# Kernel optimization log

Measured on AMD Instinct MI355X. Metric: run time of the kernel, lower is better.

Reference implementation:

```python
import jax, jax.numpy as jnp
import numpy as np

D_MODEL = 1024
NUM_HEADS = 16
SEQ_LEN = 4096
DEPTH = D_MODEL // NUM_HEADS


def setup_inputs() -> dict:
    key = jax.random.key(0)
    ks = jax.random.split(key, 11)
    sp = 1.0 / np.sqrt(D_MODEL)
    return {
        "q": jax.random.normal(ks[0], (SEQ_LEN, D_MODEL), jnp.float32),
        "k": jax.random.normal(ks[1], (SEQ_LEN, D_MODEL), jnp.float32),
        "v": jax.random.normal(ks[2], (SEQ_LEN, D_MODEL), jnp.float32),
        "Wq": jax.random.normal(ks[3], (D_MODEL, D_MODEL), jnp.float32) * sp,
        "bq": jax.random.normal(ks[4], (D_MODEL,), jnp.float32) * 0.02,
        "Wk": jax.random.normal(ks[5], (D_MODEL, D_MODEL), jnp.float32) * sp,
        "bk": jax.random.normal(ks[6], (D_MODEL,), jnp.float32) * 0.02,
        "Wv": jax.random.normal(ks[7], (D_MODEL, D_MODEL), jnp.float32) * sp,
        "bv": jax.random.normal(ks[8], (D_MODEL,), jnp.float32) * 0.02,
        "Wo": jax.random.normal(ks[9], (D_MODEL, D_MODEL), jnp.float32) * sp,
        "bo": jax.random.normal(ks[10], (D_MODEL,), jnp.float32) * 0.02,
    }


def _split_heads(x):
    # [S, D] -> [H, S, depth], matching torch reshape + permute(1,0,2)
    s = x.shape[0]
    return jnp.transpose(x.reshape(s, NUM_HEADS, DEPTH), (1, 0, 2))


def reference(q, k, v, Wq, bq, Wk, bk, Wv, bv, Wo, bo):
    # Linear projections (weights stored so that y = x @ W + b)
    qh = _split_heads(q @ Wq + bq)  # [H, S, d]
    kh = _split_heads(k @ Wk + bk)
    vh = _split_heads(v @ Wv + bv)
    scale = 1.0 / jnp.sqrt(jnp.asarray(DEPTH, qh.dtype))
    scores = jnp.einsum("hqd,hkd->hqk", qh, kh) * scale  # [H, S, S]
    attn = jax.nn.softmax(scores, axis=-1)
    vals = jnp.einsum("hqk,hkd->hqd", attn, vh)  # [H, S, d]
    concat = jnp.transpose(vals, (1, 0, 2)).reshape(q.shape[0], D_MODEL)
    out = concat @ Wo + bo
    return out, attn
```

## Files before the change

### kernel.cpp

```cpp
#include <hip/hip_runtime.h>

typedef __bf16 bf16;
typedef __attribute__((ext_vector_type(8))) __bf16 bf16x8;
typedef __attribute__((ext_vector_type(4))) float f32x4;

#define SEQ 4096
#define DM  1024
#define NH  16
#define DH  64

template<int BM, int BN, int BK, int WM, int WN, int TM, int TN,
         typename AT, typename CT>
__global__ __launch_bounds__(WM*WN*64) void gemm_bt(
    const AT* __restrict__ A, long lda, long sAb,
    const bf16* __restrict__ B, long ldb, long sBb,
    CT* __restrict__ C, long ldc, long sCb,
    const float* __restrict__ bias, float scale, int K)
{
  static_assert(BM == WM*16*TM && BN == WN*16*TN, "tile mismatch");
  constexpr int NT = WM*WN*64;
  constexpr int LDP = BK + 8;
  __shared__ bf16 As[BM][LDP];
  __shared__ bf16 Bs[BN][LDP];

  const int tid  = threadIdx.x;
  const int lane = tid & 63;
  const int wave = tid >> 6;
  const int wm   = wave % WM;
  const int wn   = wave / WM;
  const int tr   = lane & 15;
  const int quad = lane >> 4;

  A += (long)blockIdx.z * sAb + (long)blockIdx.x * BM * lda;
  B += (long)blockIdx.z * sBb + (long)blockIdx.y * BN * ldb;
  C += (long)blockIdx.z * sCb;

  f32x4 acc[TM][TN] = {};

  for (int k0 = 0; k0 < K; k0 += BK) {
    if constexpr (sizeof(AT) == 4) {
      #pragma unroll
      for (int i = tid; i < BM*(BK/4); i += NT) {
        int r = i / (BK/4), c = (i % (BK/4)) * 4;
        const float4 f = *(const float4*)(A + (long)r*lda + k0 + c);
        As[r][c+0] = (bf16)f.x; As[r][c+1] = (bf16)f.y;
        As[r][c+2] = (bf16)f.z; As[r][c+3] = (bf16)f.w;
      }
    } else {
      #pragma unroll
      for (int i = tid; i < BM*(BK/8); i += NT) {
        int r = i / (BK/8), c = (i % (BK/8)) * 8;
        *(bf16x8*)&As[r][c] = *(const bf16x8*)(A + (long)r*lda + k0 + c);
      }
    }
    #pragma unroll
    for (int i = tid; i < BN*(BK/8); i += NT) {
      int r = i / (BK/8), c = (i % (BK/8)) * 8;
      *(bf16x8*)&Bs[r][c] = *(const bf16x8*)(B + (long)r*ldb + k0 + c);
    }
    __syncthreads();

    #pragma unroll
    for (int kk = 0; kk < BK; kk += 32) {
      bf16x8 af[TM], bfr[TN];
      #pragma unroll
      for (int i = 0; i < TM; ++i)
        af[i] = *(const bf16x8*)&As[wm*16*TM + i*16 + tr][kk + quad*8];
      #pragma unroll
      for (int j = 0; j < TN; ++j)
        bfr[j] = *(const bf16x8*)&Bs[wn*16*TN + j*16 + tr][kk + quad*8];
      #pragma unroll
      for (int i = 0; i < TM; ++i)
        #pragma unroll
        for (int j = 0; j < TN; ++j)
          acc[i][j] = __builtin_amdgcn_mfma_f32_16x16x32_bf16(af[i], bfr[j], acc[i][j], 0, 0, 0);
    }
    __syncthreads();
  }

  #pragma unroll
  for (int i = 0; i < TM; ++i) {
    #pragma unroll
    for (int j = 0; j < TN; ++j) {
      const int row0 = blockIdx.x*BM + wm*16*TM + i*16 + quad*4;
      const int col  = blockIdx.y*BN + wn*16*TN + j*16 + tr;
      const float bv = bias ? bias[col] : 0.f;
      #pragma unroll
      for (int r = 0; r < 4; ++r) {
        float v = acc[i][j][r] * scale + bv;
        C[(long)(row0 + r)*ldc + col] = (CT)v;
      }
    }
  }
}

template<typename T>
__global__ void transpose_to_bf16(const T* __restrict__ src, bf16* __restrict__ dst,
                                  int R, int Cc)
{
  __shared__ T tile[32][33];
  const int c0 = blockIdx.x * 32, r0 = blockIdx.y * 32;
  const int tx = threadIdx.x, ty = threadIdx.y;
  #pragma unroll
  for (int i = ty; i < 32; i += 8)
    tile[i][tx] = src[(long)(r0 + i)*Cc + c0 + tx];
  __syncthreads();
  #pragma unroll
  for (int i = ty; i < 32; i += 8)
    dst[(long)(c0 + i)*R + r0 + tx] = (bf16)tile[tx][i];
}

__global__ __launch_bounds__(256) void softmax_rows(float* __restrict__ p)
{
  constexpr int NC = 4096;
  __shared__ float buf[NC];
  __shared__ float red[8];
  float* rp = p + (long)blockIdx.x * NC;
  const int tid = threadIdx.x;

  float lmax = -1e30f;
  #pragma unroll
  for (int i = tid; i < NC/4; i += 256) {
    float4 f = ((const float4*)rp)[i];
    ((float4*)buf)[i] = f;
    lmax = fmaxf(lmax, fmaxf(fmaxf(f.x, f.y), fmaxf(f.z, f.w)));
  }
  #pragma unroll
  for (int o = 32; o; o >>= 1) lmax = fmaxf(lmax, __shfl_xor(lmax, o, 64));
  if ((tid & 63) == 0) red[tid >> 6] = lmax;
  __syncthreads();
  const float m = fmaxf(fmaxf(red[0], red[1]), fmaxf(red[2], red[3]));

  float lsum = 0.f;
  #pragma unroll
  for (int i = tid; i < NC/4; i += 256) {
    float4 f = ((float4*)buf)[i];
    f.x = __expf(f.x - m); f.y = __expf(f.y - m);
    f.z = __expf(f.z - m); f.w = __expf(f.w - m);
    ((float4*)buf)[i] = f;
    lsum += (f.x + f.y) + (f.z + f.w);
  }
  #pragma unroll
  for (int o = 32; o; o >>= 1) lsum += __shfl_xor(lsum, o, 64);
  if ((tid & 63) == 0) red[4 + (tid >> 6)] = lsum;
  __syncthreads();
  const float inv = 1.f / (((red[4] + red[5]) + (red[6] + red[7])));

  #pragma unroll
  for (int i = tid; i < NC/4; i += 256) {
    float4 f = ((float4*)buf)[i];
    f.x *= inv; f.y *= inv; f.z *= inv; f.w *= inv;
    ((float4*)rp)[i] = f;
  }
}

extern "C" void kernel_launch(void* const* d_in, const int* in_sizes, int n_in,
                              void* d_out, int out_size, void* d_ws, size_t ws_size,
                              hipStream_t stream)
{
  const float* q  = (const float*)d_in[0];
  const float* k  = (const float*)d_in[1];
  const float* v  = (const float*)d_in[2];
  const float* Wq = (const float*)d_in[3];
  const float* bq = (const float*)d_in[4];
  const float* Wk = (const float*)d_in[5];
  const float* bk = (const float*)d_in[6];
  const float* Wv = (const float*)d_in[7];
  const float* bv = (const float*)d_in[8];
  const float* Wo = (const float*)d_in[9];
  const float* bo = (const float*)d_in[10];

  float* out  = (float*)d_out;
  float* attn = out + (long)SEQ * DM;

  char* ws = (char*)d_ws;
  bf16* WqT = (bf16*)(ws + 0l*(1l<<21));
  bf16* WkT = (bf16*)(ws + 1l*(1l<<21));
  bf16* WvT = (bf16*)(ws + 2l*(1l<<21));
  bf16* WoT = (bf16*)(ws + 3l*(1l<<21));
  bf16* Qb  = (bf16*)(ws + 1l*(1l<<23));
  bf16* Kb  = (bf16*)(ws + 2l*(1l<<23));
  bf16* Vb  = (bf16*)(ws + 3l*(1l<<23));
  bf16* Vt  = (bf16*)(ws + 4l*(1l<<23));
  bf16* Cc  = (bf16*)(ws + 5l*(1l<<23));

  const dim3 tb(32, 8);

  transpose_to_bf16<float><<<dim3(32, 32), tb, 0, stream>>>(Wq, WqT, DM, DM);
  transpose_to_bf16<float><<<dim3(32, 32), tb, 0, stream>>>(Wk, WkT, DM, DM);
  transpose_to_bf16<float><<<dim3(32, 32), tb, 0, stream>>>(Wv, WvT, DM, DM);
  transpose_to_bf16<float><<<dim3(32, 32), tb, 0, stream>>>(Wo, WoT, DM, DM);

  gemm_bt<128,128,64,2,2,4,4,float,bf16><<<dim3(32, 8, 1), 256, 0, stream>>>(
      q, DM, 0, WqT, DM, 0, Qb, DM, 0, bq, 1.f, DM);
  gemm_bt<128,128,64,2,2,4,4,float,bf16><<<dim3(32, 8, 1), 256, 0, stream>>>(
      k, DM, 0, WkT, DM, 0, Kb, DM, 0, bk, 1.f, DM);
  gemm_bt<128,128,64,2,2,4,4,float,bf16><<<dim3(32, 8, 1), 256, 0, stream>>>(
      v, DM, 0, WvT, DM, 0, Vb, DM, 0, bv, 1.f, DM);

  transpose_to_bf16<bf16><<<dim3(DM/32, SEQ/32), tb, 0, stream>>>(Vb, Vt, SEQ, DM);

  gemm_bt<128,128,64,2,2,4,4,bf16,float><<<dim3(32, 32, NH), 256, 0, stream>>>(
      Qb, DM, DH, Kb, DM, DH, attn, SEQ, (long)SEQ*SEQ, nullptr, 0.125f, DH);

  softmax_rows<<<NH*SEQ, 256, 0, stream>>>(attn);

  gemm_bt<128,64,64,2,2,4,2,float,bf16><<<dim3(32, 1, NH), 256, 0, stream>>>(
      attn, SEQ, (long)SEQ*SEQ, Vt, SEQ, (long)DH*SEQ, Cc, DM, DH, nullptr, 1.f, SEQ);

  gemm_bt<128,128,64,2,2,4,4,bf16,float><<<dim3(32, 8, 1), 256, 0, stream>>>(
      Cc, DM, 0, WoT, DM, 0, out, DM, 0, bo, 1.f, DM);
}
```

Measured before the change: 2.235 ms.

## Fuse QK^T, softmax and PV into a two-pass flash-style attention kernel

Replaces the separate score GEMM, row softmax and attn@V GEMM with one kernel per (query block, head). A first pass computes QK^T and online row max/sum statistics. A second pass recomputes the scores, writes the normalized probabilities to the attn output once, and accumulates P@V from shared memory. This removes the extra reads and writes of the 1 GB fp32 attention matrix that softmax and the PV GEMM did, at the cost of computing QK^T twice and storing attn with a non-vectorized, strided pattern.

```diff
diff --git a/kernel.cpp b/kernel.cpp
--- a/kernel.cpp
+++ b/kernel.cpp
@@ -110,47 +110,210 @@
     dst[(long)(c0 + i)*R + r0 + tx] = (bf16)tile[tx][i];
 }
 
-__global__ __launch_bounds__(256) void softmax_rows(float* __restrict__ p)
+__global__ __launch_bounds__(256) void fused_attn(
+    const bf16* __restrict__ Qb,
+    const bf16* __restrict__ Kb,
+    const bf16* __restrict__ Vt,
+    float* __restrict__ attn,
+    bf16* __restrict__ Cc)
 {
-  constexpr int NC = 4096;
-  __shared__ float buf[NC];
-  __shared__ float red[8];
-  float* rp = p + (long)blockIdx.x * NC;
-  const int tid = threadIdx.x;
-
-  float lmax = -1e30f;
-  #pragma unroll
-  for (int i = tid; i < NC/4; i += 256) {
-    float4 f = ((const float4*)rp)[i];
-    ((float4*)buf)[i] = f;
-    lmax = fmaxf(lmax, fmaxf(fmaxf(f.x, f.y), fmaxf(f.z, f.w)));
-  }
-  #pragma unroll
-  for (int o = 32; o; o >>= 1) lmax = fmaxf(lmax, __shfl_xor(lmax, o, 64));
-  if ((tid & 63) == 0) red[tid >> 6] = lmax;
+  constexpr int BM = 64;
+  constexpr int BN = 128;
+  constexpr int NTILE = SEQ / BN;
+
+  __shared__ bf16 Qs[BM][72];
+  __shared__ bf16 Ks[BN][72];
+  __shared__ bf16 Vs[DH][136];
+  __shared__ bf16 Ps[BM][136];
+  __shared__ float Msh[2][BM];
+  __shared__ float Lsh[2][BM];
+
+  const int tid  = threadIdx.x;
+  const int lane = tid & 63;
+  const int wave = tid >> 6;
+  const int wm   = wave & 1;
+  const int wn   = wave >> 1;
+  const int tr   = lane & 15;
+  const int quad = lane >> 4;
+
+  const int h  = blockIdx.y;
+  const int qb = blockIdx.x;
+
+  const bf16* Qg = Qb + (long)(qb*BM)*DM + h*DH;
+  const bf16* Kg = Kb + h*DH;
+  const bf16* Vg = Vt + (long)(h*DH)*SEQ;
+  float* attng   = attn + (long)h*SEQ*SEQ + (long)(qb*BM)*SEQ;
+
+  #pragma unroll
+  for (int i = tid; i < BM*8; i += 256) {
+    int r = i >> 3, c = (i & 7) * 8;
+    bf16x8 vv = *(const bf16x8*)(Qg + (long)r*DM + c);
+    #pragma unroll
+    for (int e = 0; e < 8; ++e) vv[e] = (bf16)((float)vv[e] * 0.125f);
+    *(bf16x8*)&Qs[r][c] = vv;
+  }
+
+  float m_[2][4], l_[2][4];
+  #pragma unroll
+  for (int ii = 0; ii < 2; ++ii)
+    #pragma unroll
+    for (int r = 0; r < 4; ++r) { m_[ii][r] = -1e30f; l_[ii][r] = 0.f; }
+
+  for (int kb = 0; kb < NTILE; ++kb) {
+    #pragma unroll
+    for (int i = tid; i < BN*8; i += 256) {
+      int r = i >> 3, c = (i & 7) * 8;
+      *(bf16x8*)&Ks[r][c] = *(const bf16x8*)(Kg + (long)(kb*BN + r)*DM + c);
+    }
+    __syncthreads();
+
+    f32x4 acc[2][4] = {};
+    #pragma unroll
+    for (int kk = 0; kk < DH; kk += 32) {
+      bf16x8 af[2], bfr[4];
+      #pragma unroll
+      for (int ii = 0; ii < 2; ++ii)
+        af[ii] = *(const bf16x8*)&Qs[wm*32 + ii*16 + tr][kk + quad*8];
+      #pragma unroll
+      for (int j = 0; j < 4; ++j)
+        bfr[j] = *(const bf16x8*)&Ks[wn*64 + j*16 + tr][kk + quad*8];
+      #pragma unroll
+      for (int ii = 0; ii < 2; ++ii)
+        #pragma unroll
+        for (int j = 0; j < 4; ++j)
+          acc[ii][j] = __builtin_amdgcn_mfma_f32_16x16x32_bf16(af[ii], bfr[j], acc[ii][j], 0, 0, 0);
+    }
+    #pragma unroll
+    for (int ii = 0; ii < 2; ++ii)
+      #pragma unroll
+      for (int r = 0; r < 4; ++r) {
+        float mx = fmaxf(fmaxf(acc[ii][0][r], acc[ii][1][r]),
+                         fmaxf(acc[ii][2][r], acc[ii][3][r]));
+        float mn = fmaxf(m_[ii][r], mx);
+        float sc = __expf(m_[ii][r] - mn);
+        float s  = __expf(acc[ii][0][r] - mn) + __expf(acc[ii][1][r] - mn)
+                 + __expf(acc[ii][2][r] - mn) + __expf(acc[ii][3][r] - mn);
+        l_[ii][r] = l_[ii][r] * sc + s;
+        m_[ii][r] = mn;
+      }
+    __syncthreads();
+  }
+
+  #pragma unroll
+  for (int ii = 0; ii < 2; ++ii)
+    #pragma unroll
+    for (int r = 0; r < 4; ++r) {
+      float mv = m_[ii][r], lv = l_[ii][r];
+      #pragma unroll
+      for (int o = 1; o <= 8; o <<= 1) {
+        float m2 = __shfl_xor(mv, o, 64);
+        float l2 = __shfl_xor(lv, o, 64);
+        float mo = fmaxf(mv, m2);
+        lv = lv * __expf(mv - mo) + l2 * __expf(m2 - mo);
+        mv = mo;
+      }
+      m_[ii][r] = mv; l_[ii][r] = lv;
+    }
+  if (tr == 0) {
+    #pragma unroll
+    for (int ii = 0; ii < 2; ++ii)
+      #pragma unroll
+      for (int r = 0; r < 4; ++r) {
+        int row = wm*32 + ii*16 + quad*4 + r;
+        Msh[wn][row] = m_[ii][r];
+        Lsh[wn][row] = l_[ii][r];
+      }
+  }
   __syncthreads();
-  const float m = fmaxf(fmaxf(red[0], red[1]), fmaxf(red[2], red[3]));
-
-  float lsum = 0.f;
-  #pragma unroll
-  for (int i = tid; i < NC/4; i += 256) {
-    float4 f = ((float4*)buf)[i];
-    f.x = __expf(f.x - m); f.y = __expf(f.y - m);
-    f.z = __expf(f.z - m); f.w = __expf(f.w - m);
-    ((float4*)buf)[i] = f;
-    lsum += (f.x + f.y) + (f.z + f.w);
-  }
-  #pragma unroll
-  for (int o = 32; o; o >>= 1) lsum += __shfl_xor(lsum, o, 64);
-  if ((tid & 63) == 0) red[4 + (tid >> 6)] = lsum;
-  __syncthreads();
-  const float inv = 1.f / (((red[4] + red[5]) + (red[6] + red[7])));
-
-  #pragma unroll
-  for (int i = tid; i < NC/4; i += 256) {
-    float4 f = ((float4*)buf)[i];
-    f.x *= inv; f.y *= inv; f.z *= inv; f.w *= inv;
-    ((float4*)rp)[i] = f;
+  float linv[2][4];
+  #pragma unroll
+  for (int ii = 0; ii < 2; ++ii)
+    #pragma unroll
+    for (int r = 0; r < 4; ++r) {
+      int row = wm*32 + ii*16 + quad*4 + r;
+      float ma = Msh[0][row], mb = Msh[1][row];
+      float mo = fmaxf(ma, mb);
+      float lt = Lsh[0][row] * __expf(ma - mo) + Lsh[1][row] * __expf(mb - mo);
+      m_[ii][r]  = mo;
+      linv[ii][r] = 1.f / lt;
+    }
+
+  f32x4 oacc[2][2] = {};
+  for (int kb = 0; kb < NTILE; ++kb) {
+    #pragma unroll
+    for (int i = tid; i < BN*8; i += 256) {
+      int r = i >> 3, c = (i & 7) * 8;
+      *(bf16x8*)&Ks[r][c] = *(const bf16x8*)(Kg + (long)(kb*BN + r)*DM + c);
+    }
+    #pragma unroll
+    for (int i = tid; i < DH*16; i += 256) {
+      int r = i >> 4, c = (i & 15) * 8;
+      *(bf16x8*)&Vs[r][c] = *(const bf16x8*)(Vg + (long)r*SEQ + kb*BN + c);
+    }
+    __syncthreads();
+
+    f32x4 acc[2][4] = {};
+    #pragma unroll
+    for (int kk = 0; kk < DH; kk += 32) {
+      bf16x8 af[2], bfr[4];
+      #pragma unroll
+      for (int ii = 0; ii < 2; ++ii)
+        af[ii] = *(const bf16x8*)&Qs[wm*32 + ii*16 + tr][kk + quad*8];
+      #pragma unroll
+      for (int j = 0; j < 4; ++j)
+        bfr[j] = *(const bf16x8*)&Ks[wn*64 + j*16 + tr][kk + quad*8];
+      #pragma unroll
+      for (int ii = 0; ii < 2; ++ii)
+        #pragma unroll
+        for (int j = 0; j < 4; ++j)
+          acc[ii][j] = __builtin_amdgcn_mfma_f32_16x16x32_bf16(af[ii], bfr[j], acc[ii][j], 0, 0, 0);
+    }
+
+    #pragma unroll
+    for (int ii = 0; ii < 2; ++ii) {
+      #pragma unroll
+      for (int j = 0; j < 4; ++j) {
+        const int col = wn*64 + j*16 + tr;
+        #pragma unroll
+        for (int r = 0; r < 4; ++r) {
+          const int row = wm*32 + ii*16 + quad*4 + r;
+          float p = __expf(acc[ii][j][r] - m_[ii][r]) * linv[ii][r];
+          attng[(long)row*SEQ + kb*BN + col] = p;
+          Ps[row][col] = (bf16)p;
+        }
+      }
+    }
+    __syncthreads();
+
+    #pragma unroll
+    for (int kk = 0; kk < BN; kk += 32) {
+      bf16x8 pa[2], vb[2];
+      #pragma unroll
+      for (int ii = 0; ii < 2; ++ii)
+        pa[ii] = *(const bf16x8*)&Ps[wm*32 + ii*16 + tr][kk + quad*8];
+      #pragma unroll
+      for (int jd = 0; jd < 2; ++jd)
+        vb[jd] = *(const bf16x8*)&Vs[wn*32 + jd*16 + tr][kk + quad*8];
+      #pragma unroll
+      for (int ii = 0; ii < 2; ++ii)
+        #pragma unroll
+        for (int jd = 0; jd < 2; ++jd)
+          oacc[ii][jd] = __builtin_amdgcn_mfma_f32_16x16x32_bf16(pa[ii], vb[jd], oacc[ii][jd], 0, 0, 0);
+    }
+    __syncthreads();
+  }
+
+  #pragma unroll
+  for (int ii = 0; ii < 2; ++ii) {
+    #pragma unroll
+    for (int jd = 0; jd < 2; ++jd) {
+      const int col = h*DH + wn*32 + jd*16 + tr;
+      #pragma unroll
+      for (int r = 0; r < 4; ++r) {
+        const int row = qb*BM + wm*32 + ii*16 + quad*4 + r;
+        Cc[(long)row*DM + col] = (bf16)oacc[ii][jd][r];
+      }
+    }
   }
 }
 
@@ -200,13 +363,7 @@
 
   transpose_to_bf16<bf16><<<dim3(DM/32, SEQ/32), tb, 0, stream>>>(Vb, Vt, SEQ, DM);
 
-  gemm_bt<128,128,64,2,2,4,4,bf16,float><<<dim3(32, 32, NH), 256, 0, stream>>>(
-      Qb, DM, DH, Kb, DM, DH, attn, SEQ, (long)SEQ*SEQ, nullptr, 0.125f, DH);
-
-  softmax_rows<<<NH*SEQ, 256, 0, stream>>>(attn);
-
-  gemm_bt<128,64,64,2,2,4,2,float,bf16><<<dim3(32, 1, NH), 256, 0, stream>>>(
-      attn, SEQ, (long)SEQ*SEQ, Vt, SEQ, (long)DH*SEQ, Cc, DM, DH, nullptr, 1.f, SEQ);
+  fused_attn<<<dim3(SEQ/64, NH), 256, 0, stream>>>(Qb, Kb, Vt, attn, Cc);
 
   gemm_bt<128,128,64,2,2,4,4,bf16,float><<<dim3(32, 8, 1), 256, 0, stream>>>(
       Cc, DM, 0, WoT, DM, 0, out, DM, 0, bo, 1.f, DM);
```

After: 1.882 ms. -15.8%, faster.
